# Optimization experiments

Measured on AMD Instinct MI355X. Metric: run time of the kernel, lower is better.

The kernel has to match this reference:

```python
import jax, jax.numpy as jnp
import numpy as np

STRIDE = (1, 1)
PADDING = ((1, 1), (1, 1))  # symmetric padding of 1 on H and W
DILATION = (1, 1)


def setup_inputs() -> dict:
    key = jax.random.key(0)
    k1, k2 = jax.random.split(key)
    x = jax.random.normal(k1, (32, 128, 56, 56), dtype=jnp.float32)
    weight = jax.random.normal(k2, (256, 128, 3, 3), dtype=jnp.float32) * 0.05
    return {"x": x, "weight": weight}


def reference(x, weight):
    # Faithful math of the im2col + matmul conv: identical to a standard
    # cross-correlation Conv2d with stride=1, padding=1, dilation=1, groups=1,
    # bias=False. Expressed as a single fused conv instead of the python-loop
    # gather + stacked GEMM of the original (same output values).
    out = jax.lax.conv_general_dilated(
        x, weight,
        window_strides=STRIDE,
        padding=PADDING,
        rhs_dilation=DILATION,
        dimension_numbers=("NCHW", "OIHW", "NCHW"),
        feature_group_count=1,
    )
    return out  # [B, C_out, H_out, W_out] = [32, 256, 56, 56]
```

## Files before the change

kernel.cpp:

```cpp
#include <hip/hip_runtime.h>
#include <stdint.h>


#define CIN   128
#define HW_   56
#define CO_   256
#define KSZ   1152
#define IMGHW 3136
#define HP    58
#define XT_BYTES ((size_t)32 * HP * HP * CIN * 2)
#define WP_BYTES ((size_t)CO_ * KSZ * 2)
#define WS_NEED  (XT_BYTES + WP_BYTES)

typedef __attribute__((ext_vector_type(8))) __bf16 bf16x8;
typedef __attribute__((ext_vector_type(4))) float f32x4;
typedef __attribute__((ext_vector_type(8))) unsigned short ushort8;

__device__ __forceinline__ unsigned short f2bf(float f) {
    unsigned int u = __float_as_uint(f);
    u += 0x7fffu + ((u >> 16) & 1u);
    return (unsigned short)(u >> 16);
}

__device__ __forceinline__ void gl2lds16(const void* g, void* l) {
    __builtin_amdgcn_global_load_lds(
        (const __attribute__((address_space(1))) void*)g,
        (__attribute__((address_space(3))) void*)l, 16, 0, 0);
}

__global__ void pack_weight(const float* __restrict__ w,
                            unsigned short* __restrict__ wp) {
    int idx = blockIdx.x * 256 + threadIdx.x;
    int co = idx / KSZ;
    int k  = idx - co * KSZ;
    int khkw = k >> 7;
    int ci = k & 127;
    wp[idx] = f2bf(w[(co * CIN + ci) * 9 + khkw]);
}

__global__ __launch_bounds__(256)
void xform(const float* __restrict__ x, unsigned short* __restrict__ xt) {
    const int nb = blockIdx.x;
    const int n  = nb / HP;
    const int hp = nb - n * HP;
    unsigned short* orow = xt + ((size_t)n * HP + hp) * (HP * CIN);
    const int t = threadIdx.x;

    if (hp == 0 || hp == HP - 1) {
        for (int i = t; i < (HP * CIN) / 8; i += 256)
            ((ushort8*)orow)[i] = (ushort8){0, 0, 0, 0, 0, 0, 0, 0};
        return;
    }
    const int h = hp - 1;
    __shared__ ushort2 T[CIN][31];
    {
        const int ci = t >> 1, part = t & 1;
        const float* src = x + (((size_t)n * CIN + ci) * IMGHW + h * HW_ + part * 28);
        #pragma unroll
        for (int j = 0; j < 7; ++j) {
            float4 v = *(const float4*)(src + 4 * j);
            T[ci][part * 14 + 2 * j]     = (ushort2){f2bf(v.x), f2bf(v.y)};
            T[ci][part * 14 + 2 * j + 1] = (ushort2){f2bf(v.z), f2bf(v.w)};
        }
    }
    __syncthreads();
    const int wpg = t >> 4, cig = t & 15;
    const int ci0 = cig * 8;
    for (int wp_ = wpg; wp_ < HP; wp_ += 16) {
        ushort8 v = (ushort8){0, 0, 0, 0, 0, 0, 0, 0};
        const int w_ = wp_ - 1;
        if ((unsigned)w_ < (unsigned)HW_) {
            #pragma unroll
            for (int e = 0; e < 8; ++e) {
                ushort2 p = T[ci0 + e][w_ >> 1];
                v[e] = (w_ & 1) ? p.y : p.x;
            }
        }
        *(ushort8*)(orow + wp_ * CIN + ci0) = v;
    }
}

__global__ __launch_bounds__(256, 3)
void conv97(const unsigned short* __restrict__ xt,
            const unsigned short* __restrict__ wpk,
            float* __restrict__ out)
{
    __shared__ __align__(16) char lds[2][16384];

    const int tid  = threadIdx.x;
    const int lane = tid & 63;
    const int wid  = tid >> 6;

    int bid = blockIdx.x;
    int flat = (bid & 7) * 196 + (bid >> 3);
    const int mt = flat >> 1;
    const int n0 = (flat & 1) << 7;
    const int m0 = mt << 7;

    const int lc = (tid & 7) ^ ((tid >> 3) & 7);
    uint32_t abase[2], bbase[2];
    #pragma unroll
    for (int p = 0; p < 2; ++p) {
        int r  = (((tid >> 3) + 32 * p) << 1) + (lc >> 2);
        int m  = m0 + r;
        int n  = m / IMGHW;
        int rem = m - n * IMGHW;
        int h  = rem / HW_;
        int w  = rem - h * HW_;
        abase[p] = (uint32_t)((((n * HP + h) * HP + w) << 8) + ((lc & 3) << 4));
        bbase[p] = (uint32_t)((n0 + r) * (KSZ * 2) + ((lc & 3) << 4));
    }

    const int fr = lane & 15, fg = lane >> 4;
    const int cp = (((fr & 1) << 2) | fg) ^ ((fr >> 1) & 7);
    const int wm0 = (wid >> 1) << 6;
    const int wn0 = (wid & 1) << 6;
    const int aB = (((wm0 >> 1) + (fr >> 1)) << 7) + (cp << 4);
    const int bB = 8192 + (((wn0 >> 1) + (fr >> 1)) << 7) + (cp << 4);

    const char* xtc = (const char*)xt;
    const char* wpc = (const char*)wpk;

    f32x4 acc[4][4];
    #pragma unroll
    for (int i = 0; i < 4; ++i)
        #pragma unroll
        for (int j = 0; j < 4; ++j)
            acc[i][j] = (f32x4){0.f, 0.f, 0.f, 0.f};

    auto STAGE = [&](int t, int buf) {
        int tap = t >> 2;
        int kh = (tap * 11) >> 5;
        int kw = tap - kh * 3;
        uint32_t asl = (uint32_t)(((kh * HP + kw) << 8) + ((t & 3) << 6));
        uint32_t bsl = (uint32_t)(t << 6);
        char* L = &lds[buf][0];
        gl2lds16(xtc + abase[0] + asl, L + tid * 16);
        gl2lds16(xtc + abase[1] + asl, L + 4096 + tid * 16);
        gl2lds16(wpc + bbase[0] + bsl, L + 8192 + tid * 16);
        gl2lds16(wpc + bbase[1] + bsl, L + 12288 + tid * 16);
    };

    STAGE(0, 0);
    __syncthreads();

    #pragma unroll 1
    for (int t = 0; t < 36; ++t) {
        if (t < 35) STAGE(t + 1, (t + 1) & 1);
        const char* L = &lds[t & 1][0];
        ushort8 a[4], b[4];
        #pragma unroll
        for (int nf = 0; nf < 4; ++nf)
            b[nf] = *(const ushort8*)(L + bB + nf * 1024);
        #pragma unroll
        for (int mf = 0; mf < 4; ++mf)
            a[mf] = *(const ushort8*)(L + aB + mf * 1024);
        #pragma unroll
        for (int mf = 0; mf < 4; ++mf)
            #pragma unroll
            for (int nf = 0; nf < 4; ++nf)
                acc[mf][nf] = __builtin_amdgcn_mfma_f32_16x16x32_bf16(
                    __builtin_bit_cast(bf16x8, b[nf]),
                    __builtin_bit_cast(bf16x8, a[mf]),
                    acc[mf][nf], 0, 0, 0);
        __syncthreads();
    }

    const int mwave = m0 + wm0;
    const int co0 = n0 + wn0 + (fg << 2);
    #pragma unroll
    for (int mf = 0; mf < 4; ++mf) {
        int m = mwave + mf * 16 + fr;
        int n = m / IMGHW;
        int hwr = m - n * IMGHW;
        uint32_t basem = (uint32_t)(n * (CO_ * IMGHW) + hwr);
        #pragma unroll
        for (int nf = 0; nf < 4; ++nf)
            #pragma unroll
            for (int q = 0; q < 4; ++q)
                out[basem + (uint32_t)(co0 + nf * 16 + q) * IMGHW] = acc[mf][nf][q];
    }
}

#define BM    64
#define BK    32
#define NSTEP 36
#define LDSP  40

template<bool PACKED>
__global__ __launch_bounds__(256, 2)
void conv_fb(const float* __restrict__ x,
             const float* __restrict__ wraw,
             const unsigned short* __restrict__ wp,
             float* __restrict__ out)
{
    __shared__ __align__(16) unsigned short Al[2][BM][LDSP];
    __shared__ __align__(16) unsigned short Bl[2][CO_][LDSP];

    const int tid  = threadIdx.x;
    const int lane = tid & 63;
    const int wid  = tid >> 6;

    const int mb    = blockIdx.x;
    const int n_img = mb / 49;
    const int hw0   = (mb - n_img * 49) * BM;

    const int mm = lane;
    const int hw = hw0 + mm;
    const int h  = hw / HW_;
    const int w_ = hw - h * HW_;

    const int bco  = tid >> 2;
    const int bkkg = tid & 3;

    float   aPF[8];
    ushort8 bPF[4];

    auto loadA = [&](int step) {
        int khkw = step >> 2;
        int kh = khkw / 3, kw = khkw - (khkw / 3) * 3;
        int ci0 = (step & 3) * BK + wid * 8;
        int ih = h + kh - 1, iw = w_ + kw - 1;
        bool valid = ((unsigned)ih < (unsigned)HW_) && ((unsigned)iw < (unsigned)HW_);
        const float* px = x + (((size_t)(n_img * CIN + ci0) * HW_ + ih) * HW_ + iw);
        #pragma unroll
        for (int e = 0; e < 8; ++e)
            aPF[e] = valid ? px[e * IMGHW] : 0.f;
    };
    auto writeA = [&](int buf) {
        ushort8 v;
        #pragma unroll
        for (int e = 0; e < 8; ++e) v[e] = f2bf(aPF[e]);
        *(ushort8*)&Al[buf][mm][wid * 8] = v;
    };
    auto loadB = [&](int step) {
        if (PACKED) {
            int k0 = step * BK;
            #pragma unroll
            for (int r = 0; r < 4; ++r)
                bPF[r] = *(const ushort8*)&wp[(r * 64 + bco) * KSZ + k0 + bkkg * 8];
        } else {
            int khkw = step >> 2;
            int ci0 = (step & 3) * BK + bkkg * 8;
            #pragma unroll
            for (int r = 0; r < 4; ++r) {
                int co = r * 64 + bco;
                ushort8 v;
                #pragma unroll
                for (int e = 0; e < 8; ++e)
                    v[e] = f2bf(wraw[(co * CIN + ci0 + e) * 9 + khkw]);
                bPF[r] = v;
            }
        }
    };
    auto writeB = [&](int buf) {
        #pragma unroll
        for (int r = 0; r < 4; ++r)
            *(ushort8*)&Bl[buf][r * 64 + bco][bkkg * 8] = bPF[r];
    };

    f32x4 acc[4][4];
    #pragma unroll
    for (int i = 0; i < 4; ++i)
        #pragma unroll
        for (int j = 0; j < 4; ++j)
            acc[i][j] = (f32x4){0.f, 0.f, 0.f, 0.f};

    const int frow = lane & 15;
    const int fk   = (lane >> 4) * 8;

    loadA(0); loadB(0);
    writeA(0); writeB(0);
    __syncthreads();

    for (int s = 0; s < NSTEP; ++s) {
        const int cur = s & 1;
        if (s + 1 < NSTEP) { loadA(s + 1); loadB(s + 1); }

        ushort8 aF[4], bF[4];
        #pragma unroll
        for (int i = 0; i < 4; ++i)
            aF[i] = *(const ushort8*)&Bl[cur][wid * 64 + i * 16 + frow][fk];
        #pragma unroll
        for (int j = 0; j < 4; ++j)
            bF[j] = *(const ushort8*)&Al[cur][j * 16 + frow][fk];

        #pragma unroll
        for (int i = 0; i < 4; ++i)
            #pragma unroll
            for (int j = 0; j < 4; ++j)
                acc[i][j] = __builtin_amdgcn_mfma_f32_16x16x32_bf16(
                    __builtin_bit_cast(bf16x8, aF[i]),
                    __builtin_bit_cast(bf16x8, bF[j]),
                    acc[i][j], 0, 0, 0);

        if (s + 1 < NSTEP) { writeA(cur ^ 1); writeB(cur ^ 1); }
        __syncthreads();
    }

    float* ob = out + (size_t)n_img * (CO_ * IMGHW) + hw0;
    #pragma unroll
    for (int i = 0; i < 4; ++i) {
        int co0 = wid * 64 + i * 16 + (lane >> 4) * 4;
        #pragma unroll
        for (int j = 0; j < 4; ++j) {
            int mcol = j * 16 + (lane & 15);
            #pragma unroll
            for (int q = 0; q < 4; ++q)
                ob[(size_t)(co0 + q) * IMGHW + mcol] = acc[i][j][q];
        }
    }
}

extern "C" void kernel_launch(void* const* d_in, const int* in_sizes, int n_in,
                              void* d_out, int out_size, void* d_ws, size_t ws_size,
                              hipStream_t stream) {
    (void)in_sizes; (void)n_in; (void)out_size;
    const float* x  = (const float*)d_in[0];
    const float* wt = (const float*)d_in[1];
    float* out = (float*)d_out;

    if (ws_size >= WS_NEED) {
        unsigned short* xt  = (unsigned short*)d_ws;
        unsigned short* wpk = (unsigned short*)((char*)d_ws + XT_BYTES);
        xform<<<32 * HP, 256, 0, stream>>>(x, xt);
        pack_weight<<<(CO_ * KSZ) / 256, 256, 0, stream>>>(wt, wpk);
        conv97<<<1568, 256, 0, stream>>>(xt, wpk, out);
    } else if (ws_size >= WP_BYTES) {
        unsigned short* wpk = (unsigned short*)d_ws;
        pack_weight<<<(CO_ * KSZ) / 256, 256, 0, stream>>>(wt, wpk);
        conv_fb<true><<<100352 / BM, 256, 0, stream>>>(x, wt, wpk, out);
    } else {
        conv_fb<false><<<100352 / BM, 256, 0, stream>>>(x, wt, nullptr, out);
    }
}
```

Measured before the change: 98.06 us.

## Restructure conv GEMM to 256x256 tiles with weights loaded directly to registers

Replaces the 128x128-tile conv kernel with a 512-thread kernel that computes a 256(M) x 256(Cout) tile per block, so every block covers all output channels and input patches are staged once rather than twice. Weights are repacked into an MFMA-fragment layout and read straight from global memory into registers, double-buffered across K steps of 64, while only the activation tile passes through LDS. It also adds explicit waitcnt/barrier scheduling and setprio around the MFMA bursts. The grid drops to 392 blocks of 512 threads, which risks poor load balance across CUs and high register pressure from the 32 accumulators per wave.

```diff
diff --git a/kernel.cpp b/kernel.cpp
--- a/kernel.cpp
+++ b/kernel.cpp
@@ -8,6 +8,7 @@
 #define KSZ   1152
 #define IMGHW 3136
 #define HP    58
+#define NT    18
 #define XT_BYTES ((size_t)32 * HP * HP * CIN * 2)
 #define WP_BYTES ((size_t)CO_ * KSZ * 2)
 #define WS_NEED  (XT_BYTES + WP_BYTES)
@@ -26,6 +27,21 @@
     __builtin_amdgcn_global_load_lds(
         (const __attribute__((address_space(1))) void*)g,
         (__attribute__((address_space(3))) void*)l, 16, 0, 0);
+}
+
+__global__ void pack_weight2(const float* __restrict__ w,
+                             unsigned short* __restrict__ wp2) {
+    int idx = blockIdx.x * 256 + threadIdx.x;
+    int e    = idx & 7;
+    int lane = (idx >> 3) & 63;
+    int nfg  = (idx >> 9) & 15;
+    int kh   = (idx >> 13) & 1;
+    int t    = idx >> 14;
+    int co = nfg * 16 + (lane & 15);
+    int k  = t * 64 + kh * 32 + (lane >> 4) * 8 + e;
+    int khkw = k >> 7;
+    int ci   = k & 127;
+    wp2[idx] = f2bf(w[(co * CIN + ci) * 9 + khkw]);
 }
 
 __global__ void pack_weight(const float* __restrict__ w,
@@ -80,96 +96,121 @@
     }
 }
 
-__global__ __launch_bounds__(256, 3)
-void conv97(const unsigned short* __restrict__ xt,
-            const unsigned short* __restrict__ wpk,
+__global__ __launch_bounds__(512, 2)
+void convbr(const unsigned short* __restrict__ xt,
+            const unsigned short* __restrict__ wp2,
             float* __restrict__ out)
 {
-    __shared__ __align__(16) char lds[2][16384];
+    __shared__ __align__(16) char lds[2 * 32768];
 
     const int tid  = threadIdx.x;
     const int lane = tid & 63;
     const int wid  = tid >> 6;
 
     int bid = blockIdx.x;
-    int flat = (bid & 7) * 196 + (bid >> 3);
-    const int mt = flat >> 1;
-    const int n0 = (flat & 1) << 7;
-    const int m0 = mt << 7;
+    bid = (bid & 7) * 49 + (bid >> 3);
+    const int m0 = bid << 8;
 
     const int lc = (tid & 7) ^ ((tid >> 3) & 7);
-    uint32_t abase[2], bbase[2];
-    #pragma unroll
-    for (int p = 0; p < 2; ++p) {
-        int r  = (((tid >> 3) + 32 * p) << 1) + (lc >> 2);
-        int m  = m0 + r;
-        int n  = m / IMGHW;
+    uint32_t aoff[4];
+    #pragma unroll
+    for (int q = 0; q < 4; ++q) {
+        int m = m0 + q * 64 + (tid >> 3);
+        int n = m / IMGHW;
         int rem = m - n * IMGHW;
-        int h  = rem / HW_;
-        int w  = rem - h * HW_;
-        abase[p] = (uint32_t)((((n * HP + h) * HP + w) << 8) + ((lc & 3) << 4));
-        bbase[p] = (uint32_t)((n0 + r) * (KSZ * 2) + ((lc & 3) << 4));
+        int h = rem / HW_;
+        int w = rem - h * HW_;
+        aoff[q] = (uint32_t)((((n * HP + h) * HP + w) << 8) + (lc << 4));
     }
 
     const int fr = lane & 15, fg = lane >> 4;
-    const int cp = (((fr & 1) << 2) | fg) ^ ((fr >> 1) & 7);
-    const int wm0 = (wid >> 1) << 6;
-    const int wn0 = (wid & 1) << 6;
-    const int aB = (((wm0 >> 1) + (fr >> 1)) << 7) + (cp << 4);
-    const int bB = 8192 + (((wn0 >> 1) + (fr >> 1)) << 7) + (cp << 4);
+    const int wm0 = (wid >> 2) << 7;
+    const int wn0 = (wid & 3) << 6;
+    const int aK0 = (wm0 + fr) * 128 + ((fg ^ (fr & 7)) << 4);
+    const int aK1 = (wm0 + fr) * 128 + (((4 | fg) ^ (fr & 7)) << 4);
+
+    const int nfb = (wid & 3) * 4;
+    const unsigned short* wpb = wp2 + lane * 8;
 
     const char* xtc = (const char*)xt;
-    const char* wpc = (const char*)wpk;
-
-    f32x4 acc[4][4];
-    #pragma unroll
-    for (int i = 0; i < 4; ++i)
+
+    f32x4 acc[8][4];
+    #pragma unroll
+    for (int i = 0; i < 8; ++i)
         #pragma unroll
         for (int j = 0; j < 4; ++j)
             acc[i][j] = (f32x4){0.f, 0.f, 0.f, 0.f};
 
-    auto STAGE = [&](int t, int buf) {
-        int tap = t >> 2;
-        int kh = (tap * 11) >> 5;
-        int kw = tap - kh * 3;
-        uint32_t asl = (uint32_t)(((kh * HP + kw) << 8) + ((t & 3) << 6));
-        uint32_t bsl = (uint32_t)(t << 6);
-        char* L = &lds[buf][0];
-        gl2lds16(xtc + abase[0] + asl, L + tid * 16);
-        gl2lds16(xtc + abase[1] + asl, L + 4096 + tid * 16);
-        gl2lds16(wpc + bbase[0] + bsl, L + 8192 + tid * 16);
-        gl2lds16(wpc + bbase[1] + bsl, L + 12288 + tid * 16);
-    };
-
-    STAGE(0, 0);
-    __syncthreads();
+    ushort8 bA[8], bB[8];
+
+    auto STAGE = [&](int t) {
+        const int bufo = (t & 1) * 32768;
+        int tap = t >> 1;
+        int khr = (tap * 11) >> 5;
+        int kwr = tap - khr * 3;
+        uint32_t asl = (uint32_t)(((khr * HP + kwr) << 8) + ((t & 1) << 7));
+        #pragma unroll
+        for (int q = 0; q < 4; ++q)
+            gl2lds16(xtc + aoff[q] + asl, &lds[bufo + q * 8192 + tid * 16]);
+    };
+
+    #define LOADB(B_, t) do { \
+        _Pragma("unroll") for (int kh_ = 0; kh_ < 2; ++kh_) \
+            _Pragma("unroll") for (int nf_ = 0; nf_ < 4; ++nf_) \
+                B_[kh_ * 4 + nf_] = *(const ushort8*)(wpb + \
+                    (size_t)(((t) * 32 + kh_ * 16 + nfb + nf_) * 512)); \
+    } while (0)
+
+    #define TILE(t, BCUR, BNXT) do { \
+        const int bufo_ = ((t) & 1) * 32768; \
+        const char* L_ = lds + bufo_; \
+        if ((t) + 1 < NT) { \
+            STAGE((t) + 1); \
+            __builtin_amdgcn_sched_barrier(0); \
+            LOADB(BNXT, (t) + 1); \
+        } \
+        ushort8 ar_[8]; \
+        _Pragma("unroll") for (int mf_ = 0; mf_ < 8; ++mf_) \
+            ar_[mf_] = *(const ushort8*)(L_ + aK0 + mf_ * 2048); \
+        __builtin_amdgcn_s_setprio(1); \
+        _Pragma("unroll") for (int mf_ = 0; mf_ < 8; ++mf_) \
+            _Pragma("unroll") for (int nf_ = 0; nf_ < 4; ++nf_) \
+                acc[mf_][nf_] = __builtin_amdgcn_mfma_f32_16x16x32_bf16( \
+                    __builtin_bit_cast(bf16x8, BCUR[nf_]), \
+                    __builtin_bit_cast(bf16x8, ar_[mf_]), \
+                    acc[mf_][nf_], 0, 0, 0); \
+        __builtin_amdgcn_s_setprio(0); \
+        _Pragma("unroll") for (int mf_ = 0; mf_ < 8; ++mf_) \
+            ar_[mf_] = *(const ushort8*)(L_ + aK1 + mf_ * 2048); \
+        __builtin_amdgcn_s_setprio(1); \
+        _Pragma("unroll") for (int mf_ = 0; mf_ < 8; ++mf_) \
+            _Pragma("unroll") for (int nf_ = 0; nf_ < 4; ++nf_) \
+                acc[mf_][nf_] = __builtin_amdgcn_mfma_f32_16x16x32_bf16( \
+                    __builtin_bit_cast(bf16x8, BCUR[4 + nf_]), \
+                    __builtin_bit_cast(bf16x8, ar_[mf_]), \
+                    acc[mf_][nf_], 0, 0, 0); \
+        __builtin_amdgcn_s_setprio(0); \
+        if ((t) + 1 < NT) \
+            asm volatile("s_waitcnt vmcnt(8)" ::: "memory"); \
+        __builtin_amdgcn_s_barrier(); \
+    } while (0)
+
+    STAGE(0);
+    __builtin_amdgcn_sched_barrier(0);
+    LOADB(bA, 0);
+    asm volatile("s_waitcnt vmcnt(0)" ::: "memory");
+    __builtin_amdgcn_s_barrier();
 
     #pragma unroll 1
-    for (int t = 0; t < 36; ++t) {
-        if (t < 35) STAGE(t + 1, (t + 1) & 1);
-        const char* L = &lds[t & 1][0];
-        ushort8 a[4], b[4];
-        #pragma unroll
-        for (int nf = 0; nf < 4; ++nf)
-            b[nf] = *(const ushort8*)(L + bB + nf * 1024);
-        #pragma unroll
-        for (int mf = 0; mf < 4; ++mf)
-            a[mf] = *(const ushort8*)(L + aB + mf * 1024);
-        #pragma unroll
-        for (int mf = 0; mf < 4; ++mf)
-            #pragma unroll
-            for (int nf = 0; nf < 4; ++nf)
-                acc[mf][nf] = __builtin_amdgcn_mfma_f32_16x16x32_bf16(
-                    __builtin_bit_cast(bf16x8, b[nf]),
-                    __builtin_bit_cast(bf16x8, a[mf]),
-                    acc[mf][nf], 0, 0, 0);
-        __syncthreads();
+    for (int tt = 0; tt < NT; tt += 2) {
+        TILE(tt, bA, bB);
+        TILE(tt + 1, bB, bA);
     }
 
     const int mwave = m0 + wm0;
-    const int co0 = n0 + wn0 + (fg << 2);
-    #pragma unroll
-    for (int mf = 0; mf < 4; ++mf) {
+    const int co0 = wn0 + (fg << 2);
+    #pragma unroll
+    for (int mf = 0; mf < 8; ++mf) {
         int m = mwave + mf * 16 + fr;
         int n = m / IMGHW;
         int hwr = m - n * IMGHW;
@@ -180,6 +221,8 @@
             for (int q = 0; q < 4; ++q)
                 out[basem + (uint32_t)(co0 + nf * 16 + q) * IMGHW] = acc[mf][nf][q];
     }
+    #undef LOADB
+    #undef TILE
 }
 
 #define BM    64
@@ -322,10 +365,10 @@
 
     if (ws_size >= WS_NEED) {
         unsigned short* xt  = (unsigned short*)d_ws;
-        unsigned short* wpk = (unsigned short*)((char*)d_ws + XT_BYTES);
+        unsigned short* wp2 = (unsigned short*)((char*)d_ws + XT_BYTES);
         xform<<<32 * HP, 256, 0, stream>>>(x, xt);
-        pack_weight<<<(CO_ * KSZ) / 256, 256, 0, stream>>>(wt, wpk);
-        conv97<<<1568, 256, 0, stream>>>(xt, wpk, out);
+        pack_weight2<<<(CO_ * KSZ) / 256, 256, 0, stream>>>(wt, wp2);
+        convbr<<<392, 512, 0, stream>>>(xt, wp2, out);
     } else if (ws_size >= WP_BYTES) {
         unsigned short* wpk = (unsigned short*)d_ws;
         pack_weight<<<(CO_ * KSZ) / 256, 256, 0, stream>>>(wt, wpk);
```

After: 185.6 us. +89.2%, slower.

## Enlarge conv tile to 256x128, fuse prep kernels, and add MFMA priority hints

Applied to the files above, without the earlier changes.

The GEMM tile per block doubles along M (256 rows instead of 128), so each wave computes 128x64 with 32 accumulators, giving more reuse of the weight tile and halving the grid to 784 blocks. The input transform and weight packing kernels are merged into one launch to save a kernel dispatch. The main loop swaps __syncthreads for an explicit vmcnt wait plus barrier and raises wave priority around the MFMA block. In exchange it uses more LDS and registers, cutting occupancy to 2 blocks per CU, and the fallback path now calls prep with a null xt and uses the unpacked conv variant.

```diff
diff --git a/kernel.cpp b/kernel.cpp
--- a/kernel.cpp
+++ b/kernel.cpp
@@ -8,9 +8,13 @@
 #define KSZ   1152
 #define IMGHW 3136
 #define HP    58
+#define NT    36
+#define BUFSZ 24576
 #define XT_BYTES ((size_t)32 * HP * HP * CIN * 2)
 #define WP_BYTES ((size_t)CO_ * KSZ * 2)
 #define WS_NEED  (XT_BYTES + WP_BYTES)
+#define XBLKS    (32 * HP)
+#define PBLKS    ((CO_ * KSZ) / 256)
 
 typedef __attribute__((ext_vector_type(8))) __bf16 bf16x8;
 typedef __attribute__((ext_vector_type(4))) float f32x4;
@@ -28,23 +32,21 @@
         (__attribute__((address_space(3))) void*)l, 16, 0, 0);
 }
 
-__global__ void pack_weight(const float* __restrict__ w,
-                            unsigned short* __restrict__ wp) {
-    int idx = blockIdx.x * 256 + threadIdx.x;
-    int co = idx / KSZ;
-    int k  = idx - co * KSZ;
-    int khkw = k >> 7;
-    int ci = k & 127;
-    wp[idx] = f2bf(w[(co * CIN + ci) * 9 + khkw]);
-}
-
 __global__ __launch_bounds__(256)
-void xform(const float* __restrict__ x, unsigned short* __restrict__ xt) {
+void prep(const float* __restrict__ x, unsigned short* __restrict__ xt,
+          const float* __restrict__ w, unsigned short* __restrict__ wp) {
+    const int t = threadIdx.x;
+    if (blockIdx.x >= XBLKS) {
+        int idx = (blockIdx.x - XBLKS) * 256 + t;
+        int co = idx / KSZ;
+        int k  = idx - co * KSZ;
+        wp[idx] = f2bf(w[(co * CIN + (k & 127)) * 9 + (k >> 7)]);
+        return;
+    }
     const int nb = blockIdx.x;
     const int n  = nb / HP;
     const int hp = nb - n * HP;
     unsigned short* orow = xt + ((size_t)n * HP + hp) * (HP * CIN);
-    const int t = threadIdx.x;
 
     if (hp == 0 || hp == HP - 1) {
         for (int i = t; i < (HP * CIN) / 8; i += 256)
@@ -80,96 +82,108 @@
     }
 }
 
-__global__ __launch_bounds__(256, 3)
-void conv97(const unsigned short* __restrict__ xt,
+__global__ __launch_bounds__(256, 2)
+void conv12(const unsigned short* __restrict__ xt,
             const unsigned short* __restrict__ wpk,
             float* __restrict__ out)
 {
-    __shared__ __align__(16) char lds[2][16384];
+    __shared__ __align__(16) char lds[2][BUFSZ];
 
     const int tid  = threadIdx.x;
     const int lane = tid & 63;
     const int wid  = tid >> 6;
 
     int bid = blockIdx.x;
-    int flat = (bid & 7) * 196 + (bid >> 3);
+    int flat = (bid & 7) * 98 + (bid >> 3);
     const int mt = flat >> 1;
     const int n0 = (flat & 1) << 7;
-    const int m0 = mt << 7;
+    const int m0 = mt << 8;
 
     const int lc = (tid & 7) ^ ((tid >> 3) & 7);
-    uint32_t abase[2], bbase[2];
-    #pragma unroll
-    for (int p = 0; p < 2; ++p) {
-        int r  = (((tid >> 3) + 32 * p) << 1) + (lc >> 2);
-        int m  = m0 + r;
-        int n  = m / IMGHW;
+    uint32_t aoff[4], boff[2];
+    #pragma unroll
+    for (int p = 0; p < 4; ++p) {
+        int m = m0 + ((p * 32 + (tid >> 3)) << 1) + (lc >> 2);
+        int n = m / IMGHW;
         int rem = m - n * IMGHW;
-        int h  = rem / HW_;
-        int w  = rem - h * HW_;
-        abase[p] = (uint32_t)((((n * HP + h) * HP + w) << 8) + ((lc & 3) << 4));
-        bbase[p] = (uint32_t)((n0 + r) * (KSZ * 2) + ((lc & 3) << 4));
+        int h = rem / HW_;
+        int w = rem - h * HW_;
+        aoff[p] = (uint32_t)((((n * HP + h) * HP + w) << 8) + ((lc & 3) << 4));
+    }
+    #pragma unroll
+    for (int q = 0; q < 2; ++q) {
+        int co = n0 + ((q * 32 + (tid >> 3)) << 1) + (lc >> 2);
+        boff[q] = (uint32_t)(co * (KSZ * 2) + ((lc & 3) << 4));
     }
 
     const int fr = lane & 15, fg = lane >> 4;
     const int cp = (((fr & 1) << 2) | fg) ^ ((fr >> 1) & 7);
-    const int wm0 = (wid >> 1) << 6;
+    const int wm0 = (wid >> 1) << 7;
     const int wn0 = (wid & 1) << 6;
     const int aB = (((wm0 >> 1) + (fr >> 1)) << 7) + (cp << 4);
-    const int bB = 8192 + (((wn0 >> 1) + (fr >> 1)) << 7) + (cp << 4);
+    const int bB = 16384 + (((wn0 >> 1) + (fr >> 1)) << 7) + (cp << 4);
 
     const char* xtc = (const char*)xt;
     const char* wpc = (const char*)wpk;
 
-    f32x4 acc[4][4];
-    #pragma unroll
-    for (int i = 0; i < 4; ++i)
+    f32x4 acc[8][4];
+    #pragma unroll
+    for (int i = 0; i < 8; ++i)
         #pragma unroll
         for (int j = 0; j < 4; ++j)
             acc[i][j] = (f32x4){0.f, 0.f, 0.f, 0.f};
 
-    auto STAGE = [&](int t, int buf) {
+    auto STAGE = [&](int t) {
+        char* L = &lds[t & 1][0];
         int tap = t >> 2;
         int kh = (tap * 11) >> 5;
         int kw = tap - kh * 3;
         uint32_t asl = (uint32_t)(((kh * HP + kw) << 8) + ((t & 3) << 6));
         uint32_t bsl = (uint32_t)(t << 6);
-        char* L = &lds[buf][0];
-        gl2lds16(xtc + abase[0] + asl, L + tid * 16);
-        gl2lds16(xtc + abase[1] + asl, L + 4096 + tid * 16);
-        gl2lds16(wpc + bbase[0] + bsl, L + 8192 + tid * 16);
-        gl2lds16(wpc + bbase[1] + bsl, L + 12288 + tid * 16);
-    };
-
-    STAGE(0, 0);
-    __syncthreads();
+        #pragma unroll
+        for (int p = 0; p < 4; ++p)
+            gl2lds16(xtc + aoff[p] + asl, L + p * 4096 + tid * 16);
+        #pragma unroll
+        for (int q = 0; q < 2; ++q)
+            gl2lds16(wpc + boff[q] + bsl, L + 16384 + q * 4096 + tid * 16);
+    };
+
+    STAGE(0);
+    asm volatile("s_waitcnt vmcnt(0)" ::: "memory");
+    __builtin_amdgcn_s_barrier();
 
     #pragma unroll 1
-    for (int t = 0; t < 36; ++t) {
-        if (t < 35) STAGE(t + 1, (t + 1) & 1);
+    for (int t = 0; t < NT; ++t) {
+        if (t + 1 < NT) STAGE(t + 1);
+
         const char* L = &lds[t & 1][0];
-        ushort8 a[4], b[4];
+        ushort8 a[8], b[4];
         #pragma unroll
         for (int nf = 0; nf < 4; ++nf)
             b[nf] = *(const ushort8*)(L + bB + nf * 1024);
         #pragma unroll
-        for (int mf = 0; mf < 4; ++mf)
+        for (int mf = 0; mf < 8; ++mf)
             a[mf] = *(const ushort8*)(L + aB + mf * 1024);
-        #pragma unroll
-        for (int mf = 0; mf < 4; ++mf)
+
+        __builtin_amdgcn_s_setprio(1);
+        #pragma unroll
+        for (int mf = 0; mf < 8; ++mf)
             #pragma unroll
             for (int nf = 0; nf < 4; ++nf)
                 acc[mf][nf] = __builtin_amdgcn_mfma_f32_16x16x32_bf16(
                     __builtin_bit_cast(bf16x8, b[nf]),
                     __builtin_bit_cast(bf16x8, a[mf]),
                     acc[mf][nf], 0, 0, 0);
-        __syncthreads();
+        __builtin_amdgcn_s_setprio(0);
+
+        if (t + 1 < NT) asm volatile("s_waitcnt vmcnt(0)" ::: "memory");
+        __builtin_amdgcn_s_barrier();
     }
 
     const int mwave = m0 + wm0;
     const int co0 = n0 + wn0 + (fg << 2);
     #pragma unroll
-    for (int mf = 0; mf < 4; ++mf) {
+    for (int mf = 0; mf < 8; ++mf) {
         int m = mwave + mf * 16 + fr;
         int n = m / IMGHW;
         int hwr = m - n * IMGHW;
@@ -323,13 +337,12 @@
     if (ws_size >= WS_NEED) {
         unsigned short* xt  = (unsigned short*)d_ws;
         unsigned short* wpk = (unsigned short*)((char*)d_ws + XT_BYTES);
-        xform<<<32 * HP, 256, 0, stream>>>(x, xt);
-        pack_weight<<<(CO_ * KSZ) / 256, 256, 0, stream>>>(wt, wpk);
-        conv97<<<1568, 256, 0, stream>>>(xt, wpk, out);
+        prep<<<XBLKS + PBLKS, 256, 0, stream>>>(x, xt, wt, wpk);
+        conv12<<<784, 256, 0, stream>>>(xt, wpk, out);
     } else if (ws_size >= WP_BYTES) {
         unsigned short* wpk = (unsigned short*)d_ws;
-        pack_weight<<<(CO_ * KSZ) / 256, 256, 0, stream>>>(wt, wpk);
-        conv_fb<true><<<100352 / BM, 256, 0, stream>>>(x, wt, wpk, out);
+        prep<<<XBLKS + PBLKS, 256, 0, stream>>>(x, nullptr, wt, wpk);
+        conv_fb<false><<<100352 / BM, 256, 0, stream>>>(x, wt, nullptr, out);
     } else {
         conv_fb<false><<<100352 / BM, 256, 0, stream>>>(x, wt, nullptr, out);
     }
```

Measured after the change: 93.66 us. 1.05x faster.
